# Kernel tuning notes

Measured on AMD Instinct MI355X. Metric: run time of the kernel, lower is better.

The kernel has to match this reference:

```python
import jax, jax.numpy as jnp
import numpy as np

IN_DIMS = 1024
OUT_DIMS = 1024
N_TOKENS = 32768


def setup_inputs() -> dict:
    key = jax.random.key(0)
    k_x, k_wl0, k_wl1, k_scale, k_shift, k_noise = jax.random.split(key, 6)
    x = jax.random.normal(k_x, (N_TOKENS, IN_DIMS), dtype=jnp.float32)
    # weight_logits[..., 0]: magnitude logits, weight_logits[..., 1]: sign logits
    gain = np.sqrt(2.0)  # relu gain
    a = gain * np.sqrt(6.0 / (IN_DIMS + OUT_DIMS))
    mag_logits = jax.random.uniform(k_wl0, (OUT_DIMS, IN_DIMS), dtype=jnp.float32,
                                    minval=-a, maxval=a)  # logit(0.5)=0, so centered at 0
    sgn_logits = jax.random.uniform(k_wl1, (OUT_DIMS, IN_DIMS), dtype=jnp.float32,
                                    minval=-a, maxval=a)
    weight_logits = jnp.stack([mag_logits, sgn_logits], axis=-1)  # [O, I, 2]
    scale = jnp.full((OUT_DIMS,), np.float32(a), dtype=jnp.float32)
    shift = jnp.full((OUT_DIMS,), 0.01, dtype=jnp.float32)
    noise = jax.random.normal(k_noise, (N_TOKENS, OUT_DIMS), dtype=jnp.float32)
    return {"x": x, "weight_logits": weight_logits, "scale": scale,
            "shift": shift, "noise": noise}


def reference(x, weight_logits, scale, shift, noise):
    # train_forward of TernaryLinear
    weight_p = jax.nn.sigmoid(weight_logits)          # [O, I, 2]
    p_mag = weight_p[..., 0]                          # P(|w| = 1)
    p_sgn = weight_p[..., 1]                          # P(w > 0 | |w| = 1)
    s = 2.0 * p_sgn - 1.0
    weight_mean = p_mag * s                           # [O, I]
    weight_var = p_mag - (p_mag * p_mag) * (s * s)    # [O, I], >= 0
    out_mean = jnp.einsum('ni,oi->no', x, weight_mean)         # [N, O]
    out_var = jnp.einsum('ni,oi->no', x * x, weight_var)       # [N, O]
    out = out_mean + jnp.sqrt(out_var) * noise
    out = out * scale[None, :] + shift[None, :]
    return out
```

## Files before the change

kernel.cpp:

```cpp
#include <hip/hip_runtime.h>
#include <hip/hip_bf16.h>
#include <cmath>

#define N_TOK 32768
#define KDIM  1024
#define ODIM  1024

#define BM 256
#define BN 128
#define BK 64
#define NKT (KDIM / BK)
#define THREADS 512
#define BUFSZ 65536

typedef float          f32x4  __attribute__((ext_vector_type(4)));
typedef __bf16         bf16x8 __attribute__((ext_vector_type(8)));
typedef unsigned short us8    __attribute__((ext_vector_type(8)));
typedef unsigned short us2   __attribute__((ext_vector_type(2)));

static __device__ __forceinline__ unsigned short f2bf(float f) {
  unsigned u = __builtin_bit_cast(unsigned, f);
  u += 0x7FFFu + ((u >> 16) & 1u);
  return (unsigned short)(u >> 16);
}

static __device__ __forceinline__ unsigned short bfc(float f) {
  return __builtin_bit_cast(unsigned short, (__bf16)f);
}

static __device__ __forceinline__ f32x4 mfma16(us8 a, us8 b, f32x4 c) {
  return __builtin_amdgcn_mfma_f32_16x16x32_bf16(
      __builtin_bit_cast(bf16x8, a), __builtin_bit_cast(bf16x8, b), c, 0, 0, 0);
}

static __device__ __forceinline__ void gl_lds16(const void* g, void* l) {
  __builtin_amdgcn_global_load_lds(
      (const __attribute__((address_space(1))) void*)g,
      (__attribute__((address_space(3))) void*)l, 16, 0, 0);
}

static __device__ __forceinline__ us8 sqr8(us8 a) {
  us8 r;
#pragma unroll
  for (int i = 0; i < 8; ++i) {
    float f = __builtin_bit_cast(float, (unsigned)a[i] << 16);
    r[i] = bfc(f * f);
  }
  return r;
}

__global__ void wprep_kernel(const float* __restrict__ wl,
                             unsigned short* __restrict__ wm,
                             unsigned short* __restrict__ wv) {
  int i = blockIdx.x * blockDim.x + threadIdx.x;
  f32x4 v = *reinterpret_cast<const f32x4*>(wl + (size_t)i * 4);
  float pm0 = 1.f / (1.f + expf(-v.x));
  float ps0 = 1.f / (1.f + expf(-v.y));
  float pm1 = 1.f / (1.f + expf(-v.z));
  float ps1 = 1.f / (1.f + expf(-v.w));
  float m0 = pm0 * (2.f * ps0 - 1.f);
  float m1 = pm1 * (2.f * ps1 - 1.f);
  float q0 = pm0 - m0 * m0;
  float q1 = pm1 - m1 * m1;
  us2 am = {f2bf(m0), f2bf(m1)};
  us2 av = {f2bf(q0), f2bf(q1)};
  *reinterpret_cast<us2*>(wm + (size_t)i * 2) = am;
  *reinterpret_cast<us2*>(wv + (size_t)i * 2) = av;
}

__global__ __launch_bounds__(THREADS, 2) void ternary_gemm(
    const float* __restrict__ x,
    const unsigned short* __restrict__ wm,
    const unsigned short* __restrict__ wv,
    const float* __restrict__ scale,
    const float* __restrict__ shift,
    const float* __restrict__ noise,
    float* __restrict__ out) {
  __shared__ alignas(16) char smem[2 * BUFSZ];

  const int tid  = threadIdx.x;
  const int lane = tid & 63;
  const int w    = tid >> 6;
  const bool isVar = (w >= 4);
  const int p    = w & 3;
  const int wr   = p >> 1;
  const int wc   = p & 1;
  const int l15  = lane & 15;
  const int l4   = lane >> 4;

  const int bid = blockIdx.x;
  const int swz = (bid & 7) * 128 + (bid >> 3);
  const int bm  = swz >> 3;
  const int bn  = swz & 7;
  const int rowBase = bm * BM;
  const int colBase = bn * BN;

  f32x4 acc[8][4];
#pragma unroll
  for (int i = 0; i < 8; ++i)
#pragma unroll
    for (int j = 0; j < 4; ++j) acc[i][j] = (f32x4)0.f;

  const float* xb = x + (size_t)rowBase * KDIM;

  auto stageB = [&](int kt, char* buf) {
    const int k0 = kt * BK;
    char* BsM = buf + 32768;
    char* BsV = buf + 49152;
#pragma unroll
    for (int c = 0; c < 2; ++c) {
      int flat = c * THREADS + tid;
      int row  = flat >> 3;
      int j    = flat & 7;
      size_t goff = (size_t)(colBase + row) * KDIM + k0 + ((j ^ (row & 7)) << 3);
      gl_lds16(wm + goff, BsM + flat * 16);
      gl_lds16(wv + goff, BsV + flat * 16);
    }
  };
  auto loadX = [&](int kt, f32x4* ap) {
    const float* xt = xb + kt * BK;
#pragma unroll
    for (int c = 0; c < 4; ++c) {
      int flat = c * THREADS + tid;
      int row  = flat >> 3;
      int j    = flat & 7;
      const float* s = xt + (size_t)row * KDIM + j * 8;
      ap[2 * c]     = *reinterpret_cast<const f32x4*>(s);
      ap[2 * c + 1] = *reinterpret_cast<const f32x4*>(s + 4);
    }
  };
  auto writeA = [&](const f32x4* ap, char* buf) {
#pragma unroll
    for (int c = 0; c < 4; ++c) {
      int flat = c * THREADS + tid;
      int row  = flat >> 3;
      int j    = flat & 7;
      f32x4 v0 = ap[2 * c], v1 = ap[2 * c + 1];
      us8 o = {bfc(v0.x), bfc(v0.y), bfc(v0.z), bfc(v0.w),
               bfc(v1.x), bfc(v1.y), bfc(v1.z), bfc(v1.w)};
      int off = row * 128 + ((j * 16) ^ ((row & 7) << 4));
      *reinterpret_cast<us8*>(buf + off) = o;
    }
  };

  f32x4 ap[8];
  stageB(0, smem);
  loadX(0, ap);
  writeA(ap, smem);
  __syncthreads();

  for (int kt = 0; kt < NKT; ++kt) {
    const char* cur = smem + (size_t)(kt & 1) * BUFSZ;
    char*       nxt = smem + (size_t)((kt + 1) & 1) * BUFSZ;

    if (kt + 1 < NKT) { stageB(kt + 1, nxt); loadX(kt + 1, ap); }

    const char* Ab = cur;
    const char* Bb = cur + 32768 + (isVar ? 16384 : 0);
#pragma unroll
    for (int ks = 0; ks < 2; ++ks) {
      const int kb = ks * 64 + (l4 << 4);
      us8 bf_[4], af[8];
#pragma unroll
      for (int b = 0; b < 4; ++b) {
        int row = wc * 64 + b * 16 + l15;
        bf_[b] = *reinterpret_cast<const us8*>(Bb + row * 128 + (kb ^ ((row & 7) << 4)));
      }
#pragma unroll
      for (int i = 0; i < 8; ++i) {
        int row = wr * 128 + i * 16 + l15;
        af[i] = *reinterpret_cast<const us8*>(Ab + row * 128 + (kb ^ ((row & 7) << 4)));
        if (isVar) af[i] = sqr8(af[i]);
      }
#pragma unroll
      for (int i = 0; i < 8; ++i)
#pragma unroll
        for (int b = 0; b < 4; ++b)
          acc[i][b] = mfma16(af[i], bf_[b], acc[i][b]);
    }

    if (kt + 1 < NKT) writeA(ap, nxt);

    __syncthreads();
  }

  float* Mx = (float*)smem;
  float* Vx = (float*)(smem + 65536);
  if (!isVar) {
#pragma unroll
    for (int i = 4; i < 8; ++i)
#pragma unroll
      for (int b = 0; b < 4; ++b)
#pragma unroll
        for (int j = 0; j < 4; ++j) {
          int lr = (i - 4) * 16 + l4 * 4 + j;
          int lc = b * 16 + l15;
          Mx[(p * 64 + lr) * 64 + (lc ^ ((lr & 4) << 2))] = acc[i][b][j];
        }
  } else {
#pragma unroll
    for (int i = 0; i < 4; ++i)
#pragma unroll
      for (int b = 0; b < 4; ++b)
#pragma unroll
        for (int j = 0; j < 4; ++j) {
          int lr = i * 16 + l4 * 4 + j;
          int lc = b * 16 + l15;
          Vx[(p * 64 + lr) * 64 + (lc ^ ((lr & 4) << 2))] = acc[i][b][j];
        }
  }
  __syncthreads();

  if (!isVar) {
#pragma unroll
    for (int i = 0; i < 4; ++i)
#pragma unroll
      for (int b = 0; b < 4; ++b) {
        int col = colBase + wc * 64 + b * 16 + l15;
        float sc = scale[col], sh = shift[col];
#pragma unroll
        for (int j = 0; j < 4; ++j) {
          int lr = i * 16 + l4 * 4 + j;
          float vv = Vx[(p * 64 + lr) * 64 + ((b * 16 + l15) ^ ((lr & 4) << 2))];
          size_t idx = (size_t)(rowBase + wr * 128 + lr) * ODIM + col;
          out[idx] = fmaf(acc[i][b][j] + sqrtf(fmaxf(vv, 0.f)) * noise[idx], sc, sh);
        }
      }
  } else {
#pragma unroll
    for (int i = 4; i < 8; ++i)
#pragma unroll
      for (int b = 0; b < 4; ++b) {
        int col = colBase + wc * 64 + b * 16 + l15;
        float sc = scale[col], sh = shift[col];
#pragma unroll
        for (int j = 0; j < 4; ++j) {
          int lr = (i - 4) * 16 + l4 * 4 + j;
          float mm = Mx[(p * 64 + lr) * 64 + ((b * 16 + l15) ^ ((lr & 4) << 2))];
          size_t idx = (size_t)(rowBase + wr * 128 + 64 + lr) * ODIM + col;
          out[idx] = fmaf(mm + sqrtf(fmaxf(acc[i][b][j], 0.f)) * noise[idx], sc, sh);
        }
      }
  }
}

extern "C" void kernel_launch(void* const* d_in, const int* in_sizes, int n_in,
                              void* d_out, int out_size, void* d_ws, size_t ws_size,
                              hipStream_t stream) {
  const float* x     = (const float*)d_in[0];
  const float* wl    = (const float*)d_in[1];
  const float* scale = (const float*)d_in[2];
  const float* shift = (const float*)d_in[3];
  const float* noise = (const float*)d_in[4];
  float* out = (float*)d_out;

  unsigned short* wm = (unsigned short*)d_ws;
  unsigned short* wv = wm + (size_t)ODIM * KDIM;

  wprep_kernel<<<(ODIM * KDIM / 2) / 256, 256, 0, stream>>>(wl, wm, wv);

  ternary_gemm<<<(N_TOK / BM) * (ODIM / BN), THREADS, 0, stream>>>(
      x, wm, wv, scale, shift, noise, out);
}
```

Measured before the change: 252.0 us.

## Pre-convert x to bf16 and shrink GEMM tiles, single-buffered LDS

Adds a separate kernel that converts x to bf16 in the workspace, so the GEMM can stage A tiles straight into LDS with global_load_lds instead of loading fp32 through registers. The block tile shrinks from 256 to 128 rows, double buffering is dropped in favour of one 48KB LDS buffer with a sync per k-step, MFMA sections get raised priority, and the mean/variance exchange in the epilogue is stored as bf16. This cuts LDS use and register pressure and allows more blocks per CU. In exchange it adds an extra pass over x in memory, loses load/compute overlap within a block, and rounds the exchanged values to bf16.

```diff
diff --git a/kernel.cpp b/kernel.cpp
--- a/kernel.cpp
+++ b/kernel.cpp
@@ -6,26 +6,27 @@
 #define KDIM  1024
 #define ODIM  1024
 
-#define BM 256
+#define BM 128
 #define BN 128
 #define BK 64
 #define NKT (KDIM / BK)
 #define THREADS 512
-#define BUFSZ 65536
 
 typedef float          f32x4  __attribute__((ext_vector_type(4)));
 typedef __bf16         bf16x8 __attribute__((ext_vector_type(8)));
 typedef unsigned short us8    __attribute__((ext_vector_type(8)));
-typedef unsigned short us2   __attribute__((ext_vector_type(2)));
+typedef unsigned short us2    __attribute__((ext_vector_type(2)));
 
 static __device__ __forceinline__ unsigned short f2bf(float f) {
   unsigned u = __builtin_bit_cast(unsigned, f);
   u += 0x7FFFu + ((u >> 16) & 1u);
   return (unsigned short)(u >> 16);
 }
-
 static __device__ __forceinline__ unsigned short bfc(float f) {
   return __builtin_bit_cast(unsigned short, (__bf16)f);
+}
+static __device__ __forceinline__ float bf2f(unsigned short u) {
+  return __builtin_bit_cast(float, (unsigned)u << 16);
 }
 
 static __device__ __forceinline__ f32x4 mfma16(us8 a, us8 b, f32x4 c) {
@@ -43,7 +44,7 @@
   us8 r;
 #pragma unroll
   for (int i = 0; i < 8; ++i) {
-    float f = __builtin_bit_cast(float, (unsigned)a[i] << 16);
+    float f = bf2f(a[i]);
     r[i] = bfc(f * f);
   }
   return r;
@@ -68,15 +69,32 @@
   *reinterpret_cast<us2*>(wv + (size_t)i * 2) = av;
 }
 
+__global__ void xprep_kernel(const float* __restrict__ x,
+                             unsigned short* __restrict__ xbf) {
+  const int t = blockIdx.x * blockDim.x + threadIdx.x;
+#pragma unroll
+  for (int i = 0; i < 4; ++i) {
+    size_t c = (size_t)i * 1048576 + t;
+    const float* s = x + c * 8;
+    f32x4 v0 = *reinterpret_cast<const f32x4*>(s);
+    f32x4 v1 = *reinterpret_cast<const f32x4*>(s + 4);
+    us8 o = {bfc(v0.x), bfc(v0.y), bfc(v0.z), bfc(v0.w),
+             bfc(v1.x), bfc(v1.y), bfc(v1.z), bfc(v1.w)};
+    *reinterpret_cast<us8*>(xbf + c * 8) = o;
+  }
+}
+
+template <bool PRE>
 __global__ __launch_bounds__(THREADS, 2) void ternary_gemm(
     const float* __restrict__ x,
+    const unsigned short* __restrict__ xbf,
     const unsigned short* __restrict__ wm,
     const unsigned short* __restrict__ wv,
     const float* __restrict__ scale,
     const float* __restrict__ shift,
     const float* __restrict__ noise,
     float* __restrict__ out) {
-  __shared__ alignas(16) char smem[2 * BUFSZ];
+  __shared__ alignas(16) char smem[49152];
 
   const int tid  = threadIdx.x;
   const int lane = tid & 63;
@@ -89,131 +107,113 @@
   const int l4   = lane >> 4;
 
   const int bid = blockIdx.x;
-  const int swz = (bid & 7) * 128 + (bid >> 3);
+  const int swz = (bid & 7) * 256 + (bid >> 3);
   const int bm  = swz >> 3;
   const int bn  = swz & 7;
   const int rowBase = bm * BM;
   const int colBase = bn * BN;
 
-  f32x4 acc[8][4];
-#pragma unroll
-  for (int i = 0; i < 8; ++i)
+  f32x4 acc[4][4];
+#pragma unroll
+  for (int i = 0; i < 4; ++i)
 #pragma unroll
     for (int j = 0; j < 4; ++j) acc[i][j] = (f32x4)0.f;
 
-  const float* xb = x + (size_t)rowBase * KDIM;
-
-  auto stageB = [&](int kt, char* buf) {
+  for (int kt = 0; kt < NKT; ++kt) {
     const int k0 = kt * BK;
-    char* BsM = buf + 32768;
-    char* BsV = buf + 49152;
+
 #pragma unroll
     for (int c = 0; c < 2; ++c) {
       int flat = c * THREADS + tid;
       int row  = flat >> 3;
       int j    = flat & 7;
-      size_t goff = (size_t)(colBase + row) * KDIM + k0 + ((j ^ (row & 7)) << 3);
-      gl_lds16(wm + goff, BsM + flat * 16);
-      gl_lds16(wv + goff, BsV + flat * 16);
+      size_t go = (size_t)(colBase + row) * KDIM + k0 + ((j ^ (row & 7)) << 3);
+      gl_lds16(wm + go, smem + 16384 + flat * 16);
+      gl_lds16(wv + go, smem + 32768 + flat * 16);
     }
-  };
-  auto loadX = [&](int kt, f32x4* ap) {
-    const float* xt = xb + kt * BK;
-#pragma unroll
-    for (int c = 0; c < 4; ++c) {
-      int flat = c * THREADS + tid;
-      int row  = flat >> 3;
-      int j    = flat & 7;
-      const float* s = xt + (size_t)row * KDIM + j * 8;
-      ap[2 * c]     = *reinterpret_cast<const f32x4*>(s);
-      ap[2 * c + 1] = *reinterpret_cast<const f32x4*>(s + 4);
+    if constexpr (PRE) {
+#pragma unroll
+      for (int c = 0; c < 2; ++c) {
+        int flat = c * THREADS + tid;
+        int row  = flat >> 3;
+        int j    = flat & 7;
+        size_t go = (size_t)(rowBase + row) * KDIM + k0 + ((j ^ (row & 7)) << 3);
+        gl_lds16(xbf + go, smem + flat * 16);
+      }
+    } else {
+#pragma unroll
+      for (int c = 0; c < 2; ++c) {
+        int flat = c * THREADS + tid;
+        int row  = flat >> 3;
+        int j    = flat & 7;
+        const float* s = x + (size_t)(rowBase + row) * KDIM + k0 + j * 8;
+        f32x4 v0 = *reinterpret_cast<const f32x4*>(s);
+        f32x4 v1 = *reinterpret_cast<const f32x4*>(s + 4);
+        us8 o = {bfc(v0.x), bfc(v0.y), bfc(v0.z), bfc(v0.w),
+                 bfc(v1.x), bfc(v1.y), bfc(v1.z), bfc(v1.w)};
+        int off = row * 128 + ((j * 16) ^ ((row & 7) << 4));
+        *reinterpret_cast<us8*>(smem + off) = o;
+      }
     }
-  };
-  auto writeA = [&](const f32x4* ap, char* buf) {
-#pragma unroll
-    for (int c = 0; c < 4; ++c) {
-      int flat = c * THREADS + tid;
-      int row  = flat >> 3;
-      int j    = flat & 7;
-      f32x4 v0 = ap[2 * c], v1 = ap[2 * c + 1];
-      us8 o = {bfc(v0.x), bfc(v0.y), bfc(v0.z), bfc(v0.w),
-               bfc(v1.x), bfc(v1.y), bfc(v1.z), bfc(v1.w)};
-      int off = row * 128 + ((j * 16) ^ ((row & 7) << 4));
-      *reinterpret_cast<us8*>(buf + off) = o;
-    }
-  };
-
-  f32x4 ap[8];
-  stageB(0, smem);
-  loadX(0, ap);
-  writeA(ap, smem);
-  __syncthreads();
-
-  for (int kt = 0; kt < NKT; ++kt) {
-    const char* cur = smem + (size_t)(kt & 1) * BUFSZ;
-    char*       nxt = smem + (size_t)((kt + 1) & 1) * BUFSZ;
-
-    if (kt + 1 < NKT) { stageB(kt + 1, nxt); loadX(kt + 1, ap); }
-
-    const char* Ab = cur;
-    const char* Bb = cur + 32768 + (isVar ? 16384 : 0);
+    __syncthreads();
+
+    const char* Bb = smem + 16384 + (isVar ? 16384 : 0);
 #pragma unroll
     for (int ks = 0; ks < 2; ++ks) {
       const int kb = ks * 64 + (l4 << 4);
-      us8 bf_[4], af[8];
+      us8 bfr[4], afr[4];
 #pragma unroll
       for (int b = 0; b < 4; ++b) {
         int row = wc * 64 + b * 16 + l15;
-        bf_[b] = *reinterpret_cast<const us8*>(Bb + row * 128 + (kb ^ ((row & 7) << 4)));
-      }
-#pragma unroll
-      for (int i = 0; i < 8; ++i) {
-        int row = wr * 128 + i * 16 + l15;
-        af[i] = *reinterpret_cast<const us8*>(Ab + row * 128 + (kb ^ ((row & 7) << 4)));
-        if (isVar) af[i] = sqr8(af[i]);
-      }
-#pragma unroll
-      for (int i = 0; i < 8; ++i)
+        bfr[b] = *reinterpret_cast<const us8*>(Bb + row * 128 + (kb ^ ((row & 7) << 4)));
+      }
+#pragma unroll
+      for (int a = 0; a < 4; ++a) {
+        int row = wr * 64 + a * 16 + l15;
+        afr[a] = *reinterpret_cast<const us8*>(smem + row * 128 + (kb ^ ((row & 7) << 4)));
+        if (isVar) afr[a] = sqr8(afr[a]);
+      }
+      __builtin_amdgcn_s_setprio(1);
+#pragma unroll
+      for (int a = 0; a < 4; ++a)
 #pragma unroll
         for (int b = 0; b < 4; ++b)
-          acc[i][b] = mfma16(af[i], bf_[b], acc[i][b]);
+          acc[a][b] = mfma16(afr[a], bfr[b], acc[a][b]);
+      __builtin_amdgcn_s_setprio(0);
     }
-
-    if (kt + 1 < NKT) writeA(ap, nxt);
-
     __syncthreads();
   }
 
-  float* Mx = (float*)smem;
-  float* Vx = (float*)(smem + 65536);
+  unsigned short* MxB = (unsigned short*)smem;
+  unsigned short* VxB = (unsigned short*)(smem + 16384);
   if (!isVar) {
 #pragma unroll
-    for (int i = 4; i < 8; ++i)
+    for (int i = 2; i < 4; ++i)
 #pragma unroll
       for (int b = 0; b < 4; ++b)
 #pragma unroll
         for (int j = 0; j < 4; ++j) {
-          int lr = (i - 4) * 16 + l4 * 4 + j;
-          int lc = b * 16 + l15;
-          Mx[(p * 64 + lr) * 64 + (lc ^ ((lr & 4) << 2))] = acc[i][b][j];
+          int lr = (i - 2) * 16 + l4 * 4 + j;
+          int lc = b * 16 + l15;
+          MxB[(p * 32 + lr) * 64 + (lc ^ (((lr >> 2) & 3) << 4))] = bfc(acc[i][b][j]);
         }
   } else {
 #pragma unroll
-    for (int i = 0; i < 4; ++i)
+    for (int i = 0; i < 2; ++i)
 #pragma unroll
       for (int b = 0; b < 4; ++b)
 #pragma unroll
         for (int j = 0; j < 4; ++j) {
           int lr = i * 16 + l4 * 4 + j;
           int lc = b * 16 + l15;
-          Vx[(p * 64 + lr) * 64 + (lc ^ ((lr & 4) << 2))] = acc[i][b][j];
+          VxB[(p * 32 + lr) * 64 + (lc ^ (((lr >> 2) & 3) << 4))] = bfc(acc[i][b][j]);
         }
   }
   __syncthreads();
 
   if (!isVar) {
 #pragma unroll
-    for (int i = 0; i < 4; ++i)
+    for (int i = 0; i < 2; ++i)
 #pragma unroll
       for (int b = 0; b < 4; ++b) {
         int col = colBase + wc * 64 + b * 16 + l15;
@@ -221,23 +221,25 @@
 #pragma unroll
         for (int j = 0; j < 4; ++j) {
           int lr = i * 16 + l4 * 4 + j;
-          float vv = Vx[(p * 64 + lr) * 64 + ((b * 16 + l15) ^ ((lr & 4) << 2))];
-          size_t idx = (size_t)(rowBase + wr * 128 + lr) * ODIM + col;
+          int lc = b * 16 + l15;
+          float vv = bf2f(VxB[(p * 32 + lr) * 64 + (lc ^ (((lr >> 2) & 3) << 4))]);
+          size_t idx = (size_t)(rowBase + wr * 64 + lr) * ODIM + col;
           out[idx] = fmaf(acc[i][b][j] + sqrtf(fmaxf(vv, 0.f)) * noise[idx], sc, sh);
         }
       }
   } else {
 #pragma unroll
-    for (int i = 4; i < 8; ++i)
+    for (int i = 2; i < 4; ++i)
 #pragma unroll
       for (int b = 0; b < 4; ++b) {
         int col = colBase + wc * 64 + b * 16 + l15;
         float sc = scale[col], sh = shift[col];
 #pragma unroll
         for (int j = 0; j < 4; ++j) {
-          int lr = (i - 4) * 16 + l4 * 4 + j;
-          float mm = Mx[(p * 64 + lr) * 64 + ((b * 16 + l15) ^ ((lr & 4) << 2))];
-          size_t idx = (size_t)(rowBase + wr * 128 + 64 + lr) * ODIM + col;
+          int lr = (i - 2) * 16 + l4 * 4 + j;
+          int lc = b * 16 + l15;
+          float mm = bf2f(MxB[(p * 32 + lr) * 64 + (lc ^ (((lr >> 2) & 3) << 4))]);
+          size_t idx = (size_t)(rowBase + wr * 64 + 32 + lr) * ODIM + col;
           out[idx] = fmaf(mm + sqrtf(fmaxf(acc[i][b][j], 0.f)) * noise[idx], sc, sh);
         }
       }
@@ -254,11 +256,21 @@
   const float* noise = (const float*)d_in[4];
   float* out = (float*)d_out;
 
-  unsigned short* wm = (unsigned short*)d_ws;
-  unsigned short* wv = wm + (size_t)ODIM * KDIM;
+  unsigned short* wm  = (unsigned short*)d_ws;
+  unsigned short* wv  = wm + (size_t)ODIM * KDIM;
+  unsigned short* xbf = wv + (size_t)ODIM * KDIM;
+
+  const size_t need = 2ull * ODIM * KDIM * 2 + (size_t)N_TOK * KDIM * 2;
+  const bool pre = (ws_size >= need);
 
   wprep_kernel<<<(ODIM * KDIM / 2) / 256, 256, 0, stream>>>(wl, wm, wv);
-
-  ternary_gemm<<<(N_TOK / BM) * (ODIM / BN), THREADS, 0, stream>>>(
-      x, wm, wv, scale, shift, noise, out);
-}
+  if (pre)
+    xprep_kernel<<<4096, 256, 0, stream>>>(x, xbf);
+
+  if (pre)
+    ternary_gemm<true><<<2048, THREADS, 0, stream>>>(
+        x, xbf, wm, wv, scale, shift, noise, out);
+  else
+    ternary_gemm<false><<<2048, THREADS, 0, stream>>>(
+        x, xbf, wm, wv, scale, shift, noise, out);
+}
```

Measured after the change: 233.2 us. 1.08x faster.
